# Performance work log

Measured on AMD Instinct MI355X. Metric: run time of the kernel, lower is better.

## Reference

```python
import jax, jax.numpy as jnp
import numpy as np

NUM_KERNELS = 50
KERNEL_DIM = 5


def setup_inputs() -> dict:
    key = jax.random.key(0)
    k1, k2 = jax.random.split(key)
    B, F = 1024, 512
    x = jax.random.normal(k1, (B, F), dtype=jnp.float32)
    # glorot-uniform-ish scale for T
    fan_in, fan_out = F, NUM_KERNELS * KERNEL_DIM
    limit = float(np.sqrt(6.0 / (fan_in + fan_out)))
    T = jax.random.uniform(k2, (F, fan_out), dtype=jnp.float32, minval=-limit, maxval=limit)
    return {"x": x, "T": T}


def reference(x, T):
    B = x.shape[0]
    # M: [B, K, D]
    M = (x @ T).reshape(B, NUM_KERNELS, KERNEL_DIM)
    # pairwise diffs: [B, K, D, B]  (M[i,k,d] - M[j,k,d])
    diffs = M[:, :, :, None] - jnp.transpose(M, (1, 2, 0))[None, :, :, :]
    abs_diffs = jnp.sum(jnp.abs(diffs), axis=2)          # [B, K, B]
    minibatch_features = jnp.sum(jnp.exp(-abs_diffs), axis=2)  # [B, K]
    return jnp.concatenate([x, minibatch_features], axis=1)
```

## Files before the change

kernel.cpp:

```cpp
#include <hip/hip_runtime.h>

#define B_SZ 1024
#define F_SZ 512
#define NK   50
#define KD   5
#define C_SZ 250
#define OUTW 562
#define PLANE (C_SZ * B_SZ)
#define NT   16
#define TILE 64
#define NPAIRS 136
#define PART_ELEMS (NK * NT * B_SZ)
#define LOG2E 1.44269504088896340736f

__global__ __launch_bounds__(256) void gemm_copy_kernel(const float* __restrict__ x,
                                                        const float* __restrict__ T,
                                                        float* __restrict__ mp,
                                                        float* __restrict__ out,
                                                        int zero_feat) {
    const int t = threadIdx.x;

    if (blockIdx.x >= 512) {
        const int b = blockIdx.x - 512;
#pragma unroll
        for (int r = 0; r < 8; ++r) {
            const int row = b * 8 + r;
            const float2* src = (const float2*)(x + (size_t)row * F_SZ);
            float2* dst = (float2*)(out + (size_t)row * OUTW);
            dst[t] = src[t];
            if (zero_feat && t < NK) out[(size_t)row * OUTW + F_SZ + t] = 0.0f;
        }
        return;
    }

    const int rt = blockIdx.x;
    if (t >= C_SZ) return;
    const int r0 = rt * 2;

    float acc0 = 0.f, acc1 = 0.f;
    const float* xp = x + (size_t)r0 * F_SZ;
    const float* Tp = T + t;

#pragma unroll 16
    for (int f = 0; f < F_SZ; ++f) {
        const float tv = Tp[(size_t)f * C_SZ];
        acc0 += xp[f] * tv;
        acc1 += xp[F_SZ + f] * tv;
    }

    float2* dst = (float2*)(mp + (size_t)t * B_SZ + r0);
    *dst = make_float2(acc0 * LOG2E, acc1 * LOG2E);
}

template <bool ATOMIC>
__global__ __launch_bounds__(256) void pair_kernel(const float* __restrict__ mp,
                                                   float* __restrict__ part,
                                                   float* __restrict__ out) {
    const int bid = blockIdx.x;
    const int k = bid / NPAIRS;
    int p = bid - k * NPAIRS;
    int ti = 0;
    while (p >= NT - ti) { p -= NT - ti; ++ti; }
    const int tj = ti + p;

    const int t    = threadIdx.x;
    const int lane = t & 63;
    const int jq   = __builtin_amdgcn_readfirstlane(threadIdx.x >> 6);

    __shared__ float rowp[4][TILE];
    __shared__ float colp[4][TILE];

    const float* pk = mp + (size_t)k * (KD * B_SZ);
    const int bi = ti * TILE;
    const int bj = tj * TILE;

    float mi[KD], mj[KD];
#pragma unroll
    for (int d = 0; d < KD; ++d) {
        mi[d] = pk[d * B_SZ + bi + lane];
        mj[d] = pk[d * B_SZ + bj + lane];
    }

    const bool diag = (ti == tj);
    float acci = 0.f, accj = 0.f;

#define ESUM(mm, c0v, c1v, c2v, c3v, c4v, C)                                     \
    __builtin_amdgcn_exp2f(-(__builtin_fabsf(mm[0] - c0v.C)                      \
                           + __builtin_fabsf(mm[1] - c1v.C)                      \
                           + __builtin_fabsf(mm[2] - c2v.C)                      \
                           + __builtin_fabsf(mm[3] - c3v.C)                      \
                           + __builtin_fabsf(mm[4] - c4v.C)))

#pragma unroll
    for (int c4 = 0; c4 < 4; ++c4) {
        const int j0 = jq * 16 + c4 * 4;

        const float4 cj0 = *(const float4*)(pk + 0 * B_SZ + bj + j0);
        const float4 cj1 = *(const float4*)(pk + 1 * B_SZ + bj + j0);
        const float4 cj2 = *(const float4*)(pk + 2 * B_SZ + bj + j0);
        const float4 cj3 = *(const float4*)(pk + 3 * B_SZ + bj + j0);
        const float4 cj4 = *(const float4*)(pk + 4 * B_SZ + bj + j0);
        acci += ESUM(mi, cj0, cj1, cj2, cj3, cj4, x);
        acci += ESUM(mi, cj0, cj1, cj2, cj3, cj4, y);
        acci += ESUM(mi, cj0, cj1, cj2, cj3, cj4, z);
        acci += ESUM(mi, cj0, cj1, cj2, cj3, cj4, w);

        if (!diag) {
            const float4 ci0 = *(const float4*)(pk + 0 * B_SZ + bi + j0);
            const float4 ci1 = *(const float4*)(pk + 1 * B_SZ + bi + j0);
            const float4 ci2 = *(const float4*)(pk + 2 * B_SZ + bi + j0);
            const float4 ci3 = *(const float4*)(pk + 3 * B_SZ + bi + j0);
            const float4 ci4 = *(const float4*)(pk + 4 * B_SZ + bi + j0);
            accj += ESUM(mj, ci0, ci1, ci2, ci3, ci4, x);
            accj += ESUM(mj, ci0, ci1, ci2, ci3, ci4, y);
            accj += ESUM(mj, ci0, ci1, ci2, ci3, ci4, z);
            accj += ESUM(mj, ci0, ci1, ci2, ci3, ci4, w);
        }
    }
#undef ESUM

    rowp[jq][lane] = acci;
    if (!diag) colp[jq][lane] = accj;
    __syncthreads();

    if (t < TILE) {
        const float r = rowp[0][t] + rowp[1][t] + rowp[2][t] + rowp[3][t];
        if (ATOMIC) atomicAdd(&out[(size_t)(bi + t) * OUTW + F_SZ + k], r);
        else        part[(size_t)(k * NT + tj) * B_SZ + bi + t] = r;
    } else if (!diag && t < 2 * TILE) {
        const int l = t - TILE;
        const float c = colp[0][l] + colp[1][l] + colp[2][l] + colp[3][l];
        if (ATOMIC) atomicAdd(&out[(size_t)(bj + l) * OUTW + F_SZ + k], c);
        else        part[(size_t)(k * NT + ti) * B_SZ + bj + l] = c;
    }
}

__global__ __launch_bounds__(256) void reduce_kernel(const float* __restrict__ part,
                                                     float* __restrict__ out) {
    const int k = blockIdx.x >> 2;
    const int i = ((blockIdx.x & 3) << 8) | threadIdx.x;
    float s = 0.0f;
#pragma unroll
    for (int sp = 0; sp < NT; ++sp)
        s += part[((size_t)(k * NT + sp)) * B_SZ + i];
    out[(size_t)i * OUTW + F_SZ + k] = s;
}

extern "C" void kernel_launch(void* const* d_in, const int* in_sizes, int n_in,
                              void* d_out, int out_size, void* d_ws, size_t ws_size,
                              hipStream_t stream) {
    const float* x = (const float*)d_in[0];
    const float* T = (const float*)d_in[1];
    float* out = (float*)d_out;
    float* mp  = (float*)d_ws;
    float* part = mp + (size_t)PLANE;

    const size_t need = (size_t)(PLANE + PART_ELEMS) * 4;
    const int fast = (ws_size >= need);

    gemm_copy_kernel<<<640, 256, 0, stream>>>(x, T, mp, out, fast ? 0 : 1);

    if (fast) {
        pair_kernel<false><<<NK * NPAIRS, 256, 0, stream>>>(mp, part, out);
        reduce_kernel<<<200, 256, 0, stream>>>(part, out);
    } else {
        pair_kernel<true><<<NK * NPAIRS, 256, 0, stream>>>(mp, nullptr, out);
    }
}
```

Baseline: 40.73 us.

## Exploit pair symmetry via LDS transpose and widen GEMM rows per block

The pair kernel now computes each off-diagonal exp term once. It stores each term into a padded shared-memory tile, and column sums are read back from that tile instead of recomputing the symmetric half. This roughly halves the exp and abs-diff work for off-diagonal tiles, at the cost of LDS writes and an extra barrier. Separately, the GEMM kernel now processes 4 rows per block instead of 2, which reuses each loaded T value more but halves the number of GEMM blocks.

```diff
diff --git a/kernel.cpp b/kernel.cpp
--- a/kernel.cpp
+++ b/kernel.cpp
@@ -20,8 +20,8 @@
                                                         int zero_feat) {
     const int t = threadIdx.x;
 
-    if (blockIdx.x >= 512) {
-        const int b = blockIdx.x - 512;
+    if (blockIdx.x >= 256) {
+        const int b = blockIdx.x - 256;
 #pragma unroll
         for (int r = 0; r < 8; ++r) {
             const int row = b * 8 + r;
@@ -35,21 +35,23 @@
 
     const int rt = blockIdx.x;
     if (t >= C_SZ) return;
-    const int r0 = rt * 2;
+    const int r0 = rt * 4;
 
-    float acc0 = 0.f, acc1 = 0.f;
+    float acc[4] = {0.f, 0.f, 0.f, 0.f};
     const float* xp = x + (size_t)r0 * F_SZ;
     const float* Tp = T + t;
 
-#pragma unroll 16
+#pragma unroll 8
     for (int f = 0; f < F_SZ; ++f) {
         const float tv = Tp[(size_t)f * C_SZ];
-        acc0 += xp[f] * tv;
-        acc1 += xp[F_SZ + f] * tv;
+#pragma unroll
+        for (int r = 0; r < 4; ++r)
+            acc[r] += xp[r * F_SZ + f] * tv;
     }
 
-    float2* dst = (float2*)(mp + (size_t)t * B_SZ + r0);
-    *dst = make_float2(acc0 * LOG2E, acc1 * LOG2E);
+    float4 v = make_float4(acc[0] * LOG2E, acc[1] * LOG2E,
+                           acc[2] * LOG2E, acc[3] * LOG2E);
+    *(float4*)(mp + (size_t)t * B_SZ + r0) = v;
 }
 
 template <bool ATOMIC>
@@ -65,62 +67,53 @@
 
     const int t    = threadIdx.x;
     const int lane = t & 63;
-    const int jq   = __builtin_amdgcn_readfirstlane(threadIdx.x >> 6);
+    const int jq   = __builtin_amdgcn_readfirstlane(t >> 6);
 
+    __shared__ float et[TILE][TILE + 1];
     __shared__ float rowp[4][TILE];
     __shared__ float colp[4][TILE];
 
     const float* pk = mp + (size_t)k * (KD * B_SZ);
     const int bi = ti * TILE;
     const int bj = tj * TILE;
+    const bool diag = (ti == tj);
 
-    float mi[KD], mj[KD];
+    float mi[KD];
 #pragma unroll
-    for (int d = 0; d < KD; ++d) {
-        mi[d] = pk[d * B_SZ + bi + lane];
-        mj[d] = pk[d * B_SZ + bj + lane];
-    }
+    for (int d = 0; d < KD; ++d) mi[d] = pk[d * B_SZ + bi + lane];
 
-    const bool diag = (ti == tj);
-    float acci = 0.f, accj = 0.f;
-
-#define ESUM(mm, c0v, c1v, c2v, c3v, c4v, C)                                     \
-    __builtin_amdgcn_exp2f(-(__builtin_fabsf(mm[0] - c0v.C)                      \
-                           + __builtin_fabsf(mm[1] - c1v.C)                      \
-                           + __builtin_fabsf(mm[2] - c2v.C)                      \
-                           + __builtin_fabsf(mm[3] - c3v.C)                      \
-                           + __builtin_fabsf(mm[4] - c4v.C)))
-
+    float acci = 0.0f;
 #pragma unroll
     for (int c4 = 0; c4 < 4; ++c4) {
         const int j0 = jq * 16 + c4 * 4;
+        const float4 c0 = *(const float4*)(pk + 0 * B_SZ + bj + j0);
+        const float4 c1 = *(const float4*)(pk + 1 * B_SZ + bj + j0);
+        const float4 c2 = *(const float4*)(pk + 2 * B_SZ + bj + j0);
+        const float4 c3 = *(const float4*)(pk + 3 * B_SZ + bj + j0);
+        const float4 c4_ = *(const float4*)(pk + 4 * B_SZ + bj + j0);
+#define PAIR_ONE(C, JOFF)                                                        \
+        {                                                                        \
+            const float s = __builtin_fabsf(mi[0] - c0.C)                        \
+                          + __builtin_fabsf(mi[1] - c1.C)                        \
+                          + __builtin_fabsf(mi[2] - c2.C)                        \
+                          + __builtin_fabsf(mi[3] - c3.C)                        \
+                          + __builtin_fabsf(mi[4] - c4_.C);                      \
+            const float e = __builtin_amdgcn_exp2f(-s);                          \
+            acci += e;                                                           \
+            if (!diag) et[j0 + JOFF][lane] = e;                                  \
+        }
+        PAIR_ONE(x, 0) PAIR_ONE(y, 1) PAIR_ONE(z, 2) PAIR_ONE(w, 3)
+#undef PAIR_ONE
+    }
+    rowp[jq][lane] = acci;
+    __syncthreads();
 
-        const float4 cj0 = *(const float4*)(pk + 0 * B_SZ + bj + j0);
-        const float4 cj1 = *(const float4*)(pk + 1 * B_SZ + bj + j0);
-        const float4 cj2 = *(const float4*)(pk + 2 * B_SZ + bj + j0);
-        const float4 cj3 = *(const float4*)(pk + 3 * B_SZ + bj + j0);
-        const float4 cj4 = *(const float4*)(pk + 4 * B_SZ + bj + j0);
-        acci += ESUM(mi, cj0, cj1, cj2, cj3, cj4, x);
-        acci += ESUM(mi, cj0, cj1, cj2, cj3, cj4, y);
-        acci += ESUM(mi, cj0, cj1, cj2, cj3, cj4, z);
-        acci += ESUM(mi, cj0, cj1, cj2, cj3, cj4, w);
-
-        if (!diag) {
-            const float4 ci0 = *(const float4*)(pk + 0 * B_SZ + bi + j0);
-            const float4 ci1 = *(const float4*)(pk + 1 * B_SZ + bi + j0);
-            const float4 ci2 = *(const float4*)(pk + 2 * B_SZ + bi + j0);
-            const float4 ci3 = *(const float4*)(pk + 3 * B_SZ + bi + j0);
-            const float4 ci4 = *(const float4*)(pk + 4 * B_SZ + bi + j0);
-            accj += ESUM(mj, ci0, ci1, ci2, ci3, ci4, x);
-            accj += ESUM(mj, ci0, ci1, ci2, ci3, ci4, y);
-            accj += ESUM(mj, ci0, ci1, ci2, ci3, ci4, z);
-            accj += ESUM(mj, ci0, ci1, ci2, ci3, ci4, w);
-        }
+    if (!diag) {
+        float csum = 0.0f;
+#pragma unroll
+        for (int e = 0; e < 16; ++e) csum += et[lane][jq * 16 + e];
+        colp[jq][lane] = csum;
     }
-#undef ESUM
-
-    rowp[jq][lane] = acci;
-    if (!diag) colp[jq][lane] = accj;
     __syncthreads();
 
     if (t < TILE) {
@@ -158,7 +151,7 @@
     const size_t need = (size_t)(PLANE + PART_ELEMS) * 4;
     const int fast = (ws_size >= need);
 
-    gemm_copy_kernel<<<640, 256, 0, stream>>>(x, T, mp, out, fast ? 0 : 1);
+    gemm_copy_kernel<<<384, 256, 0, stream>>>(x, T, mp, out, fast ? 0 : 1);
 
     if (fast) {
         pair_kernel<false><<<NK * NPAIRS, 256, 0, stream>>>(mp, part, out);
```

New measurement: 36.60 us. 1.11x faster.
